# Kernel tuning notes

Hardware: AMD Instinct MI355X
Metric: run time of the kernel (lower is better)

Reference implementation:

```python
import jax, jax.numpy as jnp
import numpy as np

V, D, H, L, E = 50000, 512, 512, 4, 40000


def setup_inputs() -> dict:
    key = jax.random.key(0)
    k1, k2, k3 = jax.random.split(key, 3)
    node_embeddings = jax.random.normal(k1, (V, D), dtype=jnp.float32)
    adjacency = jax.random.randint(k2, (L, E, 2), 0, V, dtype=jnp.int32)
    W = jax.random.normal(k3, (L, D, H), dtype=jnp.float32) * (1.0 / np.sqrt(D))
    return {"node_embeddings": node_embeddings, "adjacency": adjacency, "W": W}


def reference(node_embeddings, adjacency, W):
    # adjacency: [L, E, 2] with [:, :, 0] = source node, [:, :, 1] = target node
    src = adjacency[..., 0]  # [L, E]
    tgt = adjacency[..., 1]  # [L, E]
    # Gather source states per edge and apply per-edge-type linear message fn.
    # edge_source_states: [L, E, D]; messages: [L, E, H]
    messages = jnp.einsum("led,ldh->leh", node_embeddings[src], W)
    # Scatter-aggregate (sum) all messages to their target nodes.
    num_nodes = node_embeddings.shape[0]
    aggregated = jax.ops.segment_sum(
        messages.reshape(-1, messages.shape[-1]),  # [L*E, H]
        tgt.reshape(-1),
        num_segments=num_nodes,
    )  # [V, H]
    # message_activation_before_aggregation = False -> activation after aggregation
    return jax.nn.relu(aggregated)
```

## Files before the change

kernel.cpp:

```cpp
#include <hip/hip_runtime.h>
#include <hip/hip_bf16.h>

#define NV 50000
#define VP2 50176
#define ND 512
#define NH 512
#define NL 4
#define NE 40000
#define CAP 16
#define KTOT 2048
#define NKT 64
#define NWG4 784

typedef short bf16x8 __attribute__((ext_vector_type(8)));
typedef float f32x4  __attribute__((ext_vector_type(4)));

__device__ __forceinline__ unsigned short f2bf(float f) {
    unsigned int u = __float_as_uint(f);
    u += 0x7FFFu + ((u >> 16) & 1u);
    return (unsigned short)(u >> 16);
}
__device__ __forceinline__ unsigned pack_bf2(float x, float y) {
    return (unsigned)f2bf(x) | ((unsigned)f2bf(y) << 16);
}

#define GLL16(gp, lp) __builtin_amdgcn_global_load_lds( \
    (const __attribute__((address_space(1))) void*)(gp), \
    (__attribute__((address_space(3))) void*)(lp), 16, 0, 0)

__global__ void wt2_kernel(const float* __restrict__ W, unsigned short* __restrict__ Wt2) {
    int idx = blockIdx.x * 256 + threadIdx.x;
    int l = idx >> 18;
    int r = idx & 262143;
    int k = r >> 9;
    int h = r & 511;
    Wt2[((size_t)h << 11) + (l << 9) + k] = f2bf(W[idx]);
}

__global__ void place_kernel(const int* __restrict__ adj, int* __restrict__ cnt,
                             int* __restrict__ list) {
    int i = blockIdx.x * 256 + threadIdx.x;
    int2 p = ((const int2*)adj)[i];
    int l = i / NE;
    int cell = p.y * NL + l;
    int pos = atomicAdd(&cnt[cell], 1);
    if (pos < CAP) list[cell * CAP + pos] = p.x;
}

__global__ void __launch_bounds__(256)
agg_pull(const float* __restrict__ emb, const int* __restrict__ cnt,
         const int* __restrict__ list, unsigned* __restrict__ agg2) {
    const int wid  = blockIdx.x * 4 + (threadIdx.x >> 6);
    const int lane = threadIdx.x & 63;
    const int t    = wid >> 2;
    const int l    = wid & 3;
    const int cell = wid;
    const size_t dst = (size_t)t * 1024 + l * 256 + lane;

    int n = cnt[cell]; if (n > CAP) n = CAP;
    const int* lst = list + cell * CAP;

    float2 s0 = {0.f,0.f}, s1 = {0.f,0.f}, s2 = {0.f,0.f}, s3 = {0.f,0.f};
    int j = 0;
    for (; j + 2 <= n; j += 2) {
        const float2* p0 = (const float2*)(emb + (size_t)lst[j]     * ND) + lane;
        const float2* p1 = (const float2*)(emb + (size_t)lst[j + 1] * ND) + lane;
        float2 a0 = p0[0], a1 = p0[64], a2 = p0[128], a3 = p0[192];
        float2 b0 = p1[0], b1 = p1[64], b2 = p1[128], b3 = p1[192];
        s0.x += a0.x + b0.x; s0.y += a0.y + b0.y;
        s1.x += a1.x + b1.x; s1.y += a1.y + b1.y;
        s2.x += a2.x + b2.x; s2.y += a2.y + b2.y;
        s3.x += a3.x + b3.x; s3.y += a3.y + b3.y;
    }
    if (j < n) {
        const float2* p0 = (const float2*)(emb + (size_t)lst[j] * ND) + lane;
        float2 a0 = p0[0], a1 = p0[64], a2 = p0[128], a3 = p0[192];
        s0.x += a0.x; s0.y += a0.y;  s1.x += a1.x; s1.y += a1.y;
        s2.x += a2.x; s2.y += a2.y;  s3.x += a3.x; s3.y += a3.y;
    }
    agg2[dst]       = pack_bf2(s0.x, s0.y);
    agg2[dst + 64]  = pack_bf2(s1.x, s1.y);
    agg2[dst + 128] = pack_bf2(s2.x, s2.y);
    agg2[dst + 192] = pack_bf2(s3.x, s3.y);
}

__global__ void __launch_bounds__(512, 4)
gemm32(const unsigned short* __restrict__ agg2,
       const unsigned short* __restrict__ Wt2,
       float* __restrict__ out) {
    __shared__ unsigned short s_a[2 * 256 * 32];
    __shared__ unsigned short s_b[2 * 128 * 32];

    const int orig = blockIdx.x;
    const int wgid = (orig & 7) * (NWG4 / 8) + (orig >> 3);
    const int mt = wgid >> 2, nt = wgid & 3;
    const int t0 = mt * 256, n0 = nt * 128;

    const int tid  = threadIdx.x;
    const int lane = tid & 63;
    const int wave = tid >> 6;
    const int wm   = wave >> 1;
    const int wn   = wave & 1;
    const int laneL = lane & 15, laneH = lane >> 4;

    const int rowin = lane >> 2;
    const int sx    = (lane & 3) ^ (rowin & 3) ^ ((rowin >> 2) & 3);
    const unsigned short* srcA0 = agg2 + (size_t)(t0 + (wave * 2 + 0) * 16 + rowin) * KTOT + sx * 8;
    const unsigned short* srcA1 = agg2 + (size_t)(t0 + (wave * 2 + 1) * 16 + rowin) * KTOT + sx * 8;
    const unsigned short* srcB  = Wt2  + (size_t)(n0 + wave * 16 + rowin) * KTOT + sx * 8;
    const int ldsA0 = (wave * 2 + 0) * 512 + lane * 8;
    const int ldsA1 = (wave * 2 + 1) * 512 + lane * 8;
    const int ldsB  = wave * 512 + lane * 8;

    const int rx = (laneL & 3) ^ (laneL >> 2);
    const int fa = (wm * 64 + laneL) * 32 + ((laneH ^ rx) << 3);
    const int fb = (wn * 64 + laneL) * 32 + ((laneH ^ rx) << 3);

    f32x4 acc[4][4];
#pragma unroll
    for (int mi = 0; mi < 4; ++mi)
#pragma unroll
        for (int ni = 0; ni < 4; ++ni)
            acc[mi][ni] = (f32x4){0.f, 0.f, 0.f, 0.f};

#define STAGE_T(P) do { \
    GLL16(srcA0, s_a + (P) * 8192 + ldsA0); \
    GLL16(srcA1, s_a + (P) * 8192 + ldsA1); \
    GLL16(srcB,  s_b + (P) * 4096 + ldsB);  \
    srcA0 += 32; srcA1 += 32; srcB += 32; } while (0)

#define COMPUTE_T(P) do { \
    const unsigned short* pa = s_a + (P) * 8192; \
    const unsigned short* pb = s_b + (P) * 4096; \
    bf16x8 aF[4], bF[4]; \
    _Pragma("unroll") \
    for (int ni = 0; ni < 4; ++ni) bF[ni] = *(const bf16x8*)(pb + fb + ni * 512); \
    _Pragma("unroll") \
    for (int mi = 0; mi < 4; ++mi) aF[mi] = *(const bf16x8*)(pa + fa + mi * 512); \
    _Pragma("unroll") \
    for (int mi = 0; mi < 4; ++mi) \
        _Pragma("unroll") \
        for (int ni = 0; ni < 4; ++ni) \
            acc[mi][ni] = __builtin_amdgcn_mfma_f32_16x16x32_bf16(aF[mi], bF[ni], acc[mi][ni], 0, 0, 0); \
    } while (0)

    STAGE_T(0);
    __syncthreads();

#pragma unroll 1
    for (int it = 0; it < 31; ++it) {
        STAGE_T(1); COMPUTE_T(0); __syncthreads();
        STAGE_T(0); COMPUTE_T(1); __syncthreads();
    }
    STAGE_T(1); COMPUTE_T(0); __syncthreads();
    COMPUTE_T(1);

#undef STAGE_T
#undef COMPUTE_T

#pragma unroll
    for (int mi = 0; mi < 4; ++mi) {
#pragma unroll
        for (int i = 0; i < 4; ++i) {
            int t = t0 + wm * 64 + mi * 16 + laneH * 4 + i;
            if (t < NV) {
#pragma unroll
                for (int ni = 0; ni < 4; ++ni) {
                    int h = n0 + wn * 64 + ni * 16 + laneL;
                    out[(size_t)t * NH + h] = fmaxf(acc[mi][ni][i], 0.f);
                }
            }
        }
    }
}

__global__ void wt_legacy(const float* __restrict__ W, unsigned short* __restrict__ Wt) {
    int idx = blockIdx.x * 256 + threadIdx.x;
    int l = idx >> 18;
    int r = idx & 262143;
    int k = r >> 9;
    int h = r & 511;
    Wt[(l << 18) + (h << 9) + k] = f2bf(W[idx]);
}
__global__ void __launch_bounds__(256)
legacy_msg(const float* __restrict__ emb, const int* __restrict__ adj,
           const unsigned short* __restrict__ Wt, float* __restrict__ out) {
    __shared__ bf16x8 s_a[32 * 64];
    __shared__ int s_src[32];
    __shared__ int s_tgt[32];
    const int bx = blockIdx.x;
    const int l = bx / (NE / 32);
    const int ebase = (bx % (NE / 32)) * 32;
    const int tid = threadIdx.x, lane = tid & 63, wave = tid >> 6;
    if (tid < 32) {
        int2 p = *(const int2*)(adj + ((size_t)l * NE + ebase + tid) * 2);
        s_src[tid] = p.x; s_tgt[tid] = p.y;
    }
    __syncthreads();
    {
        const int r = tid >> 3, part = tid & 7, k0 = part * 64, rxx = r & 7;
        const float* g = emb + (size_t)s_src[r] * ND + k0;
#pragma unroll
        for (int j = 0; j < 8; ++j) {
            float4 f0 = *(const float4*)(g + j * 8);
            float4 f1 = *(const float4*)(g + j * 8 + 4);
            bf16x8 v;
            v[0]=(short)f2bf(f0.x); v[1]=(short)f2bf(f0.y);
            v[2]=(short)f2bf(f0.z); v[3]=(short)f2bf(f0.w);
            v[4]=(short)f2bf(f1.x); v[5]=(short)f2bf(f1.y);
            v[6]=(short)f2bf(f1.z); v[7]=(short)f2bf(f1.w);
            int slot = (k0 >> 3) + j;
            s_a[r * 64 + (slot ^ rxx)] = v;
        }
    }
    __syncthreads();
    const int c0 = wave * 128, laneL = lane & 15, laneH = lane >> 4, arx = laneL & 7;
    f32x4 acc[2][8];
#pragma unroll
    for (int mf = 0; mf < 2; ++mf)
#pragma unroll
        for (int nf = 0; nf < 8; ++nf) acc[mf][nf] = (f32x4){0.f,0.f,0.f,0.f};
    const bf16x8* wb = (const bf16x8*)(Wt + ((size_t)l << 18));
#pragma unroll
    for (int kc = 0; kc < 16; ++kc) {
        int slot = kc * 4 + laneH;
        bf16x8 a0 = s_a[laneL * 64 + (slot ^ arx)];
        bf16x8 a1 = s_a[(16 + laneL) * 64 + (slot ^ arx)];
#pragma unroll
        for (int nf = 0; nf < 8; ++nf) {
            bf16x8 b = wb[(c0 + nf * 16 + laneL) * 64 + slot];
            acc[0][nf] = __builtin_amdgcn_mfma_f32_16x16x32_bf16(a0, b, acc[0][nf], 0, 0, 0);
            acc[1][nf] = __builtin_amdgcn_mfma_f32_16x16x32_bf16(a1, b, acc[1][nf], 0, 0, 0);
        }
    }
#pragma unroll
    for (int mf = 0; mf < 2; ++mf)
#pragma unroll
        for (int nf = 0; nf < 8; ++nf) {
            int h = c0 + nf * 16 + laneL;
#pragma unroll
            for (int i = 0; i < 4; ++i) {
                int er = mf * 16 + laneH * 4 + i;
                atomicAdd(out + (size_t)s_tgt[er] * NH + h, acc[mf][nf][i]);
            }
        }
}
__global__ void legacy_relu(float* __restrict__ o, int n4) {
    int stride = gridDim.x * blockDim.x;
    for (int i = blockIdx.x * blockDim.x + threadIdx.x; i < n4; i += stride) {
        float4 v = ((float4*)o)[i];
        v.x = fmaxf(v.x, 0.f); v.y = fmaxf(v.y, 0.f);
        v.z = fmaxf(v.z, 0.f); v.w = fmaxf(v.w, 0.f);
        ((float4*)o)[i] = v;
    }
}

extern "C" void kernel_launch(void* const* d_in, const int* in_sizes, int n_in,
                              void* d_out, int out_size, void* d_ws, size_t ws_size,
                              hipStream_t stream) {
    const float* emb = (const float*)d_in[0];
    const int*   adj = (const int*)d_in[1];
    const float* W   = (const float*)d_in[2];
    float* out = (float*)d_out;
    char* ws = (char*)d_ws;

    unsigned short* Wt2  = (unsigned short*)ws;
    int*            cnt  = (int*)(ws + 2621440);
    int*            list = (int*)(ws + 3670016);
    unsigned short* agg2 = (unsigned short*)(ws + (16u << 20));

    const size_t need = (16u << 20) + (size_t)VP2 * KTOT * 2;

    if (ws_size >= need) {
        hipMemsetAsync(cnt, 0, (size_t)VP2 * NL * sizeof(int), stream);
        wt2_kernel<<<(NL * ND * NH) / 256, 256, 0, stream>>>(W, Wt2);
        place_kernel<<<(NL * NE) / 256, 256, 0, stream>>>(adj, cnt, list);
        agg_pull<<<(VP2 * NL) / 4, 256, 0, stream>>>(emb, cnt, list, (unsigned*)agg2);
        gemm32<<<NWG4, 512, 0, stream>>>(agg2, Wt2, out);
    } else {
        hipMemsetAsync(d_out, 0, (size_t)out_size * sizeof(float), stream);
        wt_legacy<<<(NL * ND * NH) / 256, 256, 0, stream>>>(W, Wt2);
        legacy_msg<<<NL * (NE / 32), 256, 0, stream>>>(emb, adj, Wt2, out);
        legacy_relu<<<2048, 256, 0, stream>>>(out, out_size / 4);
    }
}
```

Before: 321.4 us.

## Use triple-buffered 64-wide K tiles with manual waitcnt and priority hints in GEMM

The aggregated-feature GEMM moves from a double-buffered K=32 pipeline to a triple-buffered K=64 pipeline. Loads for tile k+2 are issued while tile k computes, with explicit vmcnt waits, raw s_barrier, sched_barrier and s_setprio around the MFMA block. The LDS swizzle is reworked for 64-element rows. The aim is to hide global-to-LDS latency and halve the barrier count, at the cost of 144KB of LDS and lower occupancy (launch bounds no longer request 4 blocks).

```diff
diff --git a/kernel.cpp b/kernel.cpp
--- a/kernel.cpp
+++ b/kernel.cpp
@@ -9,8 +9,8 @@
 #define NE 40000
 #define CAP 16
 #define KTOT 2048
-#define NKT 64
-#define NWG4 784
+#define NKT 32
+#define NWG5 784
 
 typedef short bf16x8 __attribute__((ext_vector_type(8)));
 typedef float f32x4  __attribute__((ext_vector_type(4)));
@@ -27,6 +27,13 @@
 #define GLL16(gp, lp) __builtin_amdgcn_global_load_lds( \
     (const __attribute__((address_space(1))) void*)(gp), \
     (__attribute__((address_space(3))) void*)(lp), 16, 0, 0)
+
+#define SBAR   __builtin_amdgcn_s_barrier()
+#define SCHED0 __builtin_amdgcn_sched_barrier(0)
+#define PRIO1  __builtin_amdgcn_s_setprio(1)
+#define PRIO0  __builtin_amdgcn_s_setprio(0)
+#define VMCNT6 asm volatile("s_waitcnt vmcnt(6)" ::: "memory")
+#define VMCNT0 asm volatile("s_waitcnt vmcnt(0)" ::: "memory")
 
 __global__ void wt2_kernel(const float* __restrict__ W, unsigned short* __restrict__ Wt2) {
     int idx = blockIdx.x * 256 + threadIdx.x;
@@ -84,15 +91,15 @@
     agg2[dst + 192] = pack_bf2(s3.x, s3.y);
 }
 
-__global__ void __launch_bounds__(512, 4)
-gemm32(const unsigned short* __restrict__ agg2,
+__global__ void __launch_bounds__(512)
+gemm3s(const unsigned short* __restrict__ agg2,
        const unsigned short* __restrict__ Wt2,
        float* __restrict__ out) {
-    __shared__ unsigned short s_a[2 * 256 * 32];
-    __shared__ unsigned short s_b[2 * 128 * 32];
+    __shared__ unsigned short s_a[3 * 256 * 64];
+    __shared__ unsigned short s_b[3 * 128 * 64];
 
     const int orig = blockIdx.x;
-    const int wgid = (orig & 7) * (NWG4 / 8) + (orig >> 3);
+    const int wgid = (orig & 7) * (NWG5 / 8) + (orig >> 3);
     const int mt = wgid >> 2, nt = wgid & 3;
     const int t0 = mt * 256, n0 = nt * 128;
 
@@ -102,19 +109,25 @@
     const int wm   = wave >> 1;
     const int wn   = wave & 1;
     const int laneL = lane & 15, laneH = lane >> 4;
-
-    const int rowin = lane >> 2;
-    const int sx    = (lane & 3) ^ (rowin & 3) ^ ((rowin >> 2) & 3);
-    const unsigned short* srcA0 = agg2 + (size_t)(t0 + (wave * 2 + 0) * 16 + rowin) * KTOT + sx * 8;
-    const unsigned short* srcA1 = agg2 + (size_t)(t0 + (wave * 2 + 1) * 16 + rowin) * KTOT + sx * 8;
-    const unsigned short* srcB  = Wt2  + (size_t)(n0 + wave * 16 + rowin) * KTOT + sx * 8;
-    const int ldsA0 = (wave * 2 + 0) * 512 + lane * 8;
-    const int ldsA1 = (wave * 2 + 1) * 512 + lane * 8;
-    const int ldsB  = wave * 512 + lane * 8;
-
-    const int rx = (laneL & 3) ^ (laneL >> 2);
-    const int fa = (wm * 64 + laneL) * 32 + ((laneH ^ rx) << 3);
-    const int fb = (wn * 64 + laneL) * 32 + ((laneH ^ rx) << 3);
+    const int ax = laneL & 7;
+
+    const int rowin = lane >> 3;
+    const int slt   = (lane & 7) ^ rowin;
+    const unsigned short* sA[4];
+    const unsigned short* sB[2];
+    int dA[4], dB[2];
+#pragma unroll
+    for (int j = 0; j < 4; ++j) {
+        const int cb = (wave * 4 + j) * 8;
+        sA[j] = agg2 + (size_t)(t0 + cb + rowin) * KTOT + slt * 8;
+        dA[j] = cb * 64 + lane * 8;
+    }
+#pragma unroll
+    for (int j = 0; j < 2; ++j) {
+        const int cb = (wave * 2 + j) * 8;
+        sB[j] = Wt2 + (size_t)(n0 + cb + rowin) * KTOT + slt * 8;
+        dB[j] = cb * 64 + lane * 8;
+    }
 
     f32x4 acc[4][4];
 #pragma unroll
@@ -123,40 +136,109 @@
         for (int ni = 0; ni < 4; ++ni)
             acc[mi][ni] = (f32x4){0.f, 0.f, 0.f, 0.f};
 
-#define STAGE_T(P) do { \
-    GLL16(srcA0, s_a + (P) * 8192 + ldsA0); \
-    GLL16(srcA1, s_a + (P) * 8192 + ldsA1); \
-    GLL16(srcB,  s_b + (P) * 4096 + ldsB);  \
-    srcA0 += 32; srcA1 += 32; srcB += 32; } while (0)
-
-#define COMPUTE_T(P) do { \
-    const unsigned short* pa = s_a + (P) * 8192; \
-    const unsigned short* pb = s_b + (P) * 4096; \
-    bf16x8 aF[4], bF[4]; \
-    _Pragma("unroll") \
-    for (int ni = 0; ni < 4; ++ni) bF[ni] = *(const bf16x8*)(pb + fb + ni * 512); \
-    _Pragma("unroll") \
-    for (int mi = 0; mi < 4; ++mi) aF[mi] = *(const bf16x8*)(pa + fa + mi * 512); \
+    unsigned short* const a0 = s_a;
+    unsigned short* const a2 = s_a + 2 * 16384;
+    unsigned short* const b0 = s_b;
+    unsigned short* const b2 = s_b + 2 * 8192;
+
+#define STAGE(KO, BA, BB) do { \
+    GLL16(sA[0] + (KO), (BA) + dA[0]); \
+    GLL16(sA[1] + (KO), (BA) + dA[1]); \
+    GLL16(sA[2] + (KO), (BA) + dA[2]); \
+    GLL16(sA[3] + (KO), (BA) + dA[3]); \
+    GLL16(sB[0] + (KO), (BB) + dB[0]); \
+    GLL16(sB[1] + (KO), (BB) + dB[1]); } while (0)
+
+#define COMPUTE(PA, PB) do { \
+    bf16x8 aF[4][2], bF[2][2]; \
+    _Pragma("unroll") \
+    for (int ni = 0; ni < 2; ++ni) \
+        _Pragma("unroll") \
+        for (int ks = 0; ks < 2; ++ks) { \
+            const int row = wn * 64 + ni * 16 + laneL; \
+            bF[ni][ks] = *(const bf16x8*)((PB) + row * 64 + (((ks * 4 + laneH) ^ ax) << 3)); \
+        } \
+    _Pragma("unroll") \
+    for (int mi = 0; mi < 4; ++mi) \
+        _Pragma("unroll") \
+        for (int ks = 0; ks < 2; ++ks) { \
+            const int row = wm * 64 + mi * 16 + laneL; \
+            aF[mi][ks] = *(const bf16x8*)((PA) + row * 64 + (((ks * 4 + laneH) ^ ax) << 3)); \
+        } \
+    PRIO1; \
+    _Pragma("unroll") \
+    for (int mi = 0; mi < 4; ++mi) \
+        _Pragma("unroll") \
+        for (int ks = 0; ks < 2; ++ks) { \
+            acc[mi][0] = __builtin_amdgcn_mfma_f32_16x16x32_bf16(aF[mi][ks], bF[0][ks], acc[mi][0], 0, 0, 0); \
+            acc[mi][1] = __builtin_amdgcn_mfma_f32_16x16x32_bf16(aF[mi][ks], bF[1][ks], acc[mi][1], 0, 0, 0); \
+        } \
+    _Pragma("unroll") \
+    for (int mi = 0; mi < 4; ++mi) \
+        _Pragma("unroll") \
+        for (int ks = 0; ks < 2; ++ks) { \
+            const int row = wm * 64 + mi * 16 + laneL; \
+            bf16x8 aG = *(const bf16x8*)((PA) + (row + 256 - 256) * 64 + (((ks * 4 + laneH) ^ ax) << 3)); \
+            (void)aG; \
+        } \
+    PRIO0; } while (0)
+
+#undef COMPUTE
+#define COMPUTE(PA, PB) do { \
+    bf16x8 aF[4][2], bF[4][2]; \
+    _Pragma("unroll") \
+    for (int ni = 0; ni < 4; ++ni) \
+        _Pragma("unroll") \
+        for (int ks = 0; ks < 2; ++ks) { \
+            const int row = wn * 64 + ni * 16 + laneL; \
+            bF[ni][ks] = *(const bf16x8*)((PB) + row * 64 + (((ks * 4 + laneH) ^ ax) << 3)); \
+        } \
+    _Pragma("unroll") \
+    for (int mi = 0; mi < 4; ++mi) \
+        _Pragma("unroll") \
+        for (int ks = 0; ks < 2; ++ks) { \
+            const int row = wm * 64 + mi * 16 + laneL; \
+            aF[mi][ks] = *(const bf16x8*)((PA) + row * 64 + (((ks * 4 + laneH) ^ ax) << 3)); \
+        } \
+    PRIO1; \
     _Pragma("unroll") \
     for (int mi = 0; mi < 4; ++mi) \
         _Pragma("unroll") \
         for (int ni = 0; ni < 4; ++ni) \
-            acc[mi][ni] = __builtin_amdgcn_mfma_f32_16x16x32_bf16(aF[mi], bF[ni], acc[mi][ni], 0, 0, 0); \
-    } while (0)
-
-    STAGE_T(0);
-    __syncthreads();
+            _Pragma("unroll") \
+            for (int ks = 0; ks < 2; ++ks) \
+                acc[mi][ni] = __builtin_amdgcn_mfma_f32_16x16x32_bf16(aF[mi][ks], bF[ni][ks], acc[mi][ni], 0, 0, 0); \
+    PRIO0; } while (0)
+
+    STAGE(0,  a0, b0);
+    STAGE(64, a0 + 16384, b0 + 8192);
+    VMCNT6; SCHED0; SBAR;
+
+    const unsigned short* pa = a0;
+    const unsigned short* pb = b0;
+    unsigned short* qa = a2;
+    unsigned short* qb = b2;
+    int koff = 128;
 
 #pragma unroll 1
-    for (int it = 0; it < 31; ++it) {
-        STAGE_T(1); COMPUTE_T(0); __syncthreads();
-        STAGE_T(0); COMPUTE_T(1); __syncthreads();
-    }
-    STAGE_T(1); COMPUTE_T(0); __syncthreads();
-    COMPUTE_T(1);
-
-#undef STAGE_T
-#undef COMPUTE_T
+    for (int T = 0; T < 30; ++T) {
+        STAGE(koff, qa, qb);
+        koff += 64;
+        COMPUTE(pa, pb);
+        VMCNT6; SCHED0; SBAR;
+        pa = (pa == a2) ? a0 : pa + 16384;
+        pb = (pb == b2) ? b0 : pb + 8192;
+        qa = (qa == a2) ? a0 : qa + 16384;
+        qb = (qb == b2) ? b0 : qb + 8192;
+    }
+    COMPUTE(pa, pb);
+    VMCNT0; SCHED0; SBAR;
+    pa = (pa == a2) ? a0 : pa + 16384;
+    pb = (pb == b2) ? b0 : pb + 8192;
+    COMPUTE(pa, pb);
+
+#undef STAGE
+#undef COMPUTE
 
 #pragma unroll
     for (int mi = 0; mi < 4; ++mi) {
@@ -276,7 +358,7 @@
         wt2_kernel<<<(NL * ND * NH) / 256, 256, 0, stream>>>(W, Wt2);
         place_kernel<<<(NL * NE) / 256, 256, 0, stream>>>(adj, cnt, list);
         agg_pull<<<(VP2 * NL) / 4, 256, 0, stream>>>(emb, cnt, list, (unsigned*)agg2);
-        gemm32<<<NWG4, 512, 0, stream>>>(agg2, Wt2, out);
+        gemm3s<<<NWG5, 512, 0, stream>>>(agg2, Wt2, out);
     } else {
         hipMemsetAsync(d_out, 0, (size_t)out_size * sizeof(float), stream);
         wt_legacy<<<(NL * ND * NH) / 256, 256, 0, stream>>>(W, Wt2);
```

After: 344.5 us. 1.07x slower.

## Replace LDS-staged GEMM with register-direct loads over k-sliced transposed operands

Applied to the files above, without the earlier changes.

Aggregated features and weights are now stored in a k-slice-major layout (8 bf16 per row per slice), so each lane can load its MFMA fragments straight from global memory into registers. This removes LDS staging, swizzling and barriers, and the GEMM tile shrinks to 128x128 with 256 threads and twice as many workgroups. Without LDS sharing, each wave fetches its own A and B fragments from global memory and relies on L2/L1 for reuse, so global traffic rises. The agg_pull writes are also scattered with a large stride.

```diff
diff --git a/kernel.cpp b/kernel.cpp
--- a/kernel.cpp
+++ b/kernel.cpp
@@ -9,8 +9,7 @@
 #define NE 40000
 #define CAP 16
 #define KTOT 2048
-#define NKT 64
-#define NWG4 784
+#define NWG6 1568
 
 typedef short bf16x8 __attribute__((ext_vector_type(8)));
 typedef float f32x4  __attribute__((ext_vector_type(4)));
@@ -24,17 +23,17 @@
     return (unsigned)f2bf(x) | ((unsigned)f2bf(y) << 16);
 }
 
-#define GLL16(gp, lp) __builtin_amdgcn_global_load_lds( \
-    (const __attribute__((address_space(1))) void*)(gp), \
-    (__attribute__((address_space(3))) void*)(lp), 16, 0, 0)
-
-__global__ void wt2_kernel(const float* __restrict__ W, unsigned short* __restrict__ Wt2) {
+__global__ void wt2t_kernel(const float* __restrict__ W, unsigned short* __restrict__ Wt2T) {
     int idx = blockIdx.x * 256 + threadIdx.x;
-    int l = idx >> 18;
-    int r = idx & 262143;
-    int k = r >> 9;
-    int h = r & 511;
-    Wt2[((size_t)h << 11) + (l << 9) + k] = f2bf(W[idx]);
+    int l  = idx >> 15;
+    int r  = idx & 32767;
+    int ks = r >> 9;
+    int h  = r & 511;
+    const float* src = W + ((size_t)l << 18) + (size_t)ks * 8 * 512 + h;
+    bf16x8 v;
+#pragma unroll
+    for (int j = 0; j < 8; ++j) v[j] = (short)f2bf(src[(size_t)j * 512]);
+    *(bf16x8*)(Wt2T + ((size_t)(l * 64 + ks) * 512 + h) * 8) = v;
 }
 
 __global__ void place_kernel(const int* __restrict__ adj, int* __restrict__ cnt,
@@ -55,7 +54,6 @@
     const int t    = wid >> 2;
     const int l    = wid & 3;
     const int cell = wid;
-    const size_t dst = (size_t)t * 1024 + l * 256 + lane;
 
     int n = cnt[cell]; if (n > CAP) n = CAP;
     const int* lst = list + cell * CAP;
@@ -78,23 +76,22 @@
         s0.x += a0.x; s0.y += a0.y;  s1.x += a1.x; s1.y += a1.y;
         s2.x += a2.x; s2.y += a2.y;  s3.x += a3.x; s3.y += a3.y;
     }
-    agg2[dst]       = pack_bf2(s0.x, s0.y);
-    agg2[dst + 64]  = pack_bf2(s1.x, s1.y);
-    agg2[dst + 128] = pack_bf2(s2.x, s2.y);
-    agg2[dst + 192] = pack_bf2(s3.x, s3.y);
-}
-
-__global__ void __launch_bounds__(512, 4)
-gemm32(const unsigned short* __restrict__ agg2,
-       const unsigned short* __restrict__ Wt2,
-       float* __restrict__ out) {
-    __shared__ unsigned short s_a[2 * 256 * 32];
-    __shared__ unsigned short s_b[2 * 128 * 32];
-
+    const size_t dst = ((size_t)(l * 64 + (lane >> 2)) * VP2 + t) * 4 + (lane & 3);
+    const size_t stp = (size_t)VP2 * 64;
+    agg2[dst]           = pack_bf2(s0.x, s0.y);
+    agg2[dst + stp]     = pack_bf2(s1.x, s1.y);
+    agg2[dst + 2 * stp] = pack_bf2(s2.x, s2.y);
+    agg2[dst + 3 * stp] = pack_bf2(s3.x, s3.y);
+}
+
+__global__ void __launch_bounds__(256)
+gemm_reg(const unsigned short* __restrict__ agg2T,
+         const unsigned short* __restrict__ Wt2T,
+         float* __restrict__ out) {
     const int orig = blockIdx.x;
-    const int wgid = (orig & 7) * (NWG4 / 8) + (orig >> 3);
+    const int wgid = (orig & 7) * (NWG6 / 8) + (orig >> 3);
     const int mt = wgid >> 2, nt = wgid & 3;
-    const int t0 = mt * 256, n0 = nt * 128;
+    const int t0 = mt * 128, n0 = nt * 128;
 
     const int tid  = threadIdx.x;
     const int lane = tid & 63;
@@ -103,18 +100,14 @@
     const int wn   = wave & 1;
     const int laneL = lane & 15, laneH = lane >> 4;
 
-    const int rowin = lane >> 2;
-    const int sx    = (lane & 3) ^ (rowin & 3) ^ ((rowin >> 2) & 3);
-    const unsigned short* srcA0 = agg2 + (size_t)(t0 + (wave * 2 + 0) * 16 + rowin) * KTOT + sx * 8;
-    const unsigned short* srcA1 = agg2 + (size_t)(t0 + (wave * 2 + 1) * 16 + rowin) * KTOT + sx * 8;
-    const unsigned short* srcB  = Wt2  + (size_t)(n0 + wave * 16 + rowin) * KTOT + sx * 8;
-    const int ldsA0 = (wave * 2 + 0) * 512 + lane * 8;
-    const int ldsA1 = (wave * 2 + 1) * 512 + lane * 8;
-    const int ldsB  = wave * 512 + lane * 8;
-
-    const int rx = (laneL & 3) ^ (laneL >> 2);
-    const int fa = (wm * 64 + laneL) * 32 + ((laneH ^ rx) << 3);
-    const int fb = (wn * 64 + laneL) * 32 + ((laneH ^ rx) << 3);
+    const size_t ASL = (size_t)VP2 * 8;
+    const size_t BSL = 512 * 8;
+    const unsigned short* ap = agg2T + (size_t)laneH * ASL
+                             + (size_t)(t0 + wm * 64 + laneL) * 8;
+    const unsigned short* bp = Wt2T + (size_t)laneH * BSL
+                             + (size_t)(n0 + wn * 64 + laneL) * 8;
+    const size_t ainc = 4 * ASL;
+    const size_t binc = 4 * BSL;
 
     f32x4 acc[4][4];
 #pragma unroll
@@ -123,40 +116,37 @@
         for (int ni = 0; ni < 4; ++ni)
             acc[mi][ni] = (f32x4){0.f, 0.f, 0.f, 0.f};
 
-#define STAGE_T(P) do { \
-    GLL16(srcA0, s_a + (P) * 8192 + ldsA0); \
-    GLL16(srcA1, s_a + (P) * 8192 + ldsA1); \
-    GLL16(srcB,  s_b + (P) * 4096 + ldsB);  \
-    srcA0 += 32; srcA1 += 32; srcB += 32; } while (0)
-
-#define COMPUTE_T(P) do { \
-    const unsigned short* pa = s_a + (P) * 8192; \
-    const unsigned short* pb = s_b + (P) * 4096; \
-    bf16x8 aF[4], bF[4]; \
-    _Pragma("unroll") \
-    for (int ni = 0; ni < 4; ++ni) bF[ni] = *(const bf16x8*)(pb + fb + ni * 512); \
-    _Pragma("unroll") \
-    for (int mi = 0; mi < 4; ++mi) aF[mi] = *(const bf16x8*)(pa + fa + mi * 512); \
+    bf16x8 a0[4], b0[4], a1[4], b1[4];
+
+#define LOADSET(A, B) do { \
+    A[0] = *(const bf16x8*)(ap);        A[1] = *(const bf16x8*)(ap + 128); \
+    A[2] = *(const bf16x8*)(ap + 256);  A[3] = *(const bf16x8*)(ap + 384); \
+    B[0] = *(const bf16x8*)(bp);        B[1] = *(const bf16x8*)(bp + 128); \
+    B[2] = *(const bf16x8*)(bp + 256);  B[3] = *(const bf16x8*)(bp + 384); \
+    ap += ainc; bp += binc; } while (0)
+
+#define MFMASET(A, B) do { \
     _Pragma("unroll") \
     for (int mi = 0; mi < 4; ++mi) \
         _Pragma("unroll") \
         for (int ni = 0; ni < 4; ++ni) \
-            acc[mi][ni] = __builtin_amdgcn_mfma_f32_16x16x32_bf16(aF[mi], bF[ni], acc[mi][ni], 0, 0, 0); \
+            acc[mi][ni] = __builtin_amdgcn_mfma_f32_16x16x32_bf16(A[mi], B[ni], acc[mi][ni], 0, 0, 0); \
     } while (0)
 
-    STAGE_T(0);
-    __syncthreads();
-
+    LOADSET(a0, b0);
 #pragma unroll 1
     for (int it = 0; it < 31; ++it) {
-        STAGE_T(1); COMPUTE_T(0); __syncthreads();
-        STAGE_T(0); COMPUTE_T(1); __syncthreads();
-    }
-    STAGE_T(1); COMPUTE_T(0); __syncthreads();
-    COMPUTE_T(1);
-
-#undef STAGE_T
-#undef COMPUTE_T
+        LOADSET(a1, b1);
+        MFMASET(a0, b0);
+        LOADSET(a0, b0);
+        MFMASET(a1, b1);
+    }
+    LOADSET(a1, b1);
+    MFMASET(a0, b0);
+    MFMASET(a1, b1);
+
+#undef LOADSET
+#undef MFMASET
 
 #pragma unroll
     for (int mi = 0; mi < 4; ++mi) {
@@ -273,10 +263,10 @@
 
     if (ws_size >= need) {
         hipMemsetAsync(cnt, 0, (size_t)VP2 * NL * sizeof(int), stream);
-        wt2_kernel<<<(NL * ND * NH) / 256, 256, 0, stream>>>(W, Wt2);
+        wt2t_kernel<<<(NL * 64 * 512) / 256, 256, 0, stream>>>(W, Wt2);
         place_kernel<<<(NL * NE) / 256, 256, 0, stream>>>(adj, cnt, list);
         agg_pull<<<(VP2 * NL) / 4, 256, 0, stream>>>(emb, cnt, list, (unsigned*)agg2);
-        gemm32<<<NWG4, 512, 0, stream>>>(agg2, Wt2, out);
+        gemm_reg<<<NWG6, 256, 0, stream>>>(agg2, Wt2, out);
     } else {
         hipMemsetAsync(d_out, 0, (size_t)out_size * sizeof(float), stream);
         wt_legacy<<<(NL * ND * NH) / 256, 256, 0, stream>>>(W, Wt2);
```

Result: slower. 463.0 us (+44.1%).
